# Optimization experiments

Hardware: AMD Instinct MI355X
Metric: run time of the kernel (lower is better)

Reference implementation:

```python
import jax, jax.numpy as jnp
import numpy as np

B, L, K, D = 1024, 8, 16, 64
_KSCALE = 1.0 / np.sqrt(K * D)  # keep channel roughly norm-preserving over layers


def setup_inputs() -> dict:
    key = jax.random.key(0)
    k1, k2, k3, k4 = jax.random.split(key, 4)
    state_re = jax.random.normal(k1, (B, D, D), dtype=jnp.float32)
    state_im = jax.random.normal(k2, (B, D, D), dtype=jnp.float32)
    kraus_re = jax.random.normal(k3, (L, K, D, D), dtype=jnp.float32) * _KSCALE
    kraus_im = jax.random.normal(k4, (L, K, D, D), dtype=jnp.float32) * _KSCALE
    return {"state_re": state_re, "state_im": state_im,
            "kraus_re": kraus_re, "kraus_im": kraus_im}


def reference(state_re, state_im, kraus_re, kraus_im):
    # rho: [B, d, d] complex density matrices; kraus: [L, K, d, d]
    rho = (state_re + 1j * state_im).astype(jnp.complex64)
    kraus = (kraus_re + 1j * kraus_im).astype(jnp.complex64)

    def layer_step(rho, Kl):
        # Kl: [K, d, d]. output_state = sum_k  K_k @ rho @ K_k^dagger
        tmp = jnp.einsum('kij,bjl->kbil', Kl, rho)            # K_k @ rho
        rho_new = jnp.einsum('kbil,kml->bim', tmp, Kl.conj())  # (...) @ K_k^dagger, summed over k
        return rho_new, None

    rho, _ = jax.lax.scan(layer_step, rho, kraus)
    # return real/imag stacked as float32: [2, B, d, d]
    return jnp.stack([rho.real, rho.imag])
```

## Files before the change

kernel.cpp:

```cpp
#include <hip/hip_runtime.h>
#include <hip/hip_fp16.h>

#define D 64
#define NKR 16
#define NB 1024
#define NL 8

typedef __attribute__((ext_vector_type(8))) _Float16 half8;
typedef __attribute__((ext_vector_type(16))) float f32x16;
typedef __attribute__((ext_vector_type(4))) int i32x4;

static __device__ __forceinline__ half8 neg8(half8 x) {
    i32x4 u = __builtin_bit_cast(i32x4, x);
    u = u ^ (int)0x80008000;
    return __builtin_bit_cast(half8, u);
}

static __device__ __forceinline__ unsigned pkrtz(float a, float b) {
    auto h = __builtin_amdgcn_cvt_pkrtz(a, b);
    return __builtin_bit_cast(unsigned, h);
}

static __device__ __forceinline__ void plswap(unsigned &a, unsigned &b) {
    asm volatile("v_permlane32_swap_b32 %0, %1" : "+v"(a), "+v"(b));
}

union Pack4 { _Float16 h[4]; uint2 u; };
union H8 { unsigned u[4]; uint2 v[2]; half8 h; };

#define MFMA __builtin_amdgcn_mfma_f32_32x32x16_f16


__global__ void kconv_kernel(const float* __restrict__ re, const float* __restrict__ im,
                             _Float16* __restrict__ out) {
    int plane = blockIdx.y;
    int idx = blockIdx.x * blockDim.x + threadIdx.x;
    const float* src = plane ? im : re;
    float4 v = ((const float4*)src)[idx];
    int e = idx * 4;
    int lk = e >> 12;
    int rem = e & 4095;
    int row = rem >> 6, col = rem & 63;
    int ihalf = row >> 5, r31 = row & 31;
    int ks = col >> 4, hl2 = (col >> 3) & 1, c = col & 7;
    Pack4 p;
    p.h[0] = (_Float16)v.x; p.h[1] = (_Float16)v.y;
    p.h[2] = (_Float16)v.z; p.h[3] = (_Float16)v.w;
    size_t off = (size_t)(lk * 2 + plane) * 4096 + ihalf * 2048
               + (2 * ks + hl2) * 256 + r31 * 8 + c;
    *(uint2*)(out + off) = p.u;
}

__global__ void sconv_kernel(const float* __restrict__ re, const float* __restrict__ im,
                             _Float16* __restrict__ out) {
    __shared__ float tile[64][65];
    int b = blockIdx.x;
    int t = threadIdx.x;
    for (int plane = 0; plane < 2; ++plane) {
        const float* src = (plane ? im : re) + (size_t)b * 4096;
        __syncthreads();
        #pragma unroll
        for (int i = 0; i < 16; ++i) {
            int e = t + 256 * i;
            tile[e >> 6][e & 63] = src[e];
        }
        __syncthreads();
        _Float16* o = out + ((size_t)b * 2 + plane) * 4096;
        #pragma unroll
        for (int i = 0; i < 16; ++i) {
            int oi = t + 256 * i;
            int lh = oi >> 11, slot = (oi >> 8) & 7, r = (oi >> 3) & 31, c = oi & 7;
            int col = 16 * (slot >> 1) + 8 * (slot & 1) + c;
            int row = 32 * lh + r;
            o[oi] = (_Float16)tile[col][row];
        }
    }
}

static __device__ __forceinline__ void exchange(const f32x16 &dd, half8 &f0, half8 &f1) {
    unsigned A0 = pkrtz(dd[0],  dd[1]),  B0 = pkrtz(dd[2],  dd[3]);
    unsigned A1 = pkrtz(dd[4],  dd[5]),  B1 = pkrtz(dd[6],  dd[7]);
    unsigned A2 = pkrtz(dd[8],  dd[9]),  B2 = pkrtz(dd[10], dd[11]);
    unsigned A3 = pkrtz(dd[12], dd[13]), B3 = pkrtz(dd[14], dd[15]);
    plswap(A0, A1);
    plswap(B0, B1);
    plswap(A2, A3);
    plswap(B2, B3);
    H8 h0; h0.u[0] = A0; h0.u[1] = B0; h0.u[2] = A1; h0.u[3] = B1; f0 = h0.h;
    H8 h1; h1.u[0] = A2; h1.u[1] = B2; h1.u[2] = A3; h1.u[3] = B3; f1 = h1.h;
}

template<int IT>
static __device__ __forceinline__ void kstep(
    const _Float16* __restrict__ kb,
    const _Float16* __restrict__ rb,
    f32x16 (&accRe)[2], f32x16 (&accIm)[2],
    int lane)
{
    const _Float16* bo = kb + IT * 2048;
    const _Float16* bx = kb + (1 - IT) * 2048;

    half8 bre[4], bim[4];
    #pragma unroll
    for (int ks = 0; ks < 4; ++ks) {
        bre[ks] = *(const half8*)(bo + ks * 512 + lane * 8);
        bim[ks] = *(const half8*)(bo + 4096 + ks * 512 + lane * 8);
    }

    half8 ar0 = *(const half8*)(rb + lane * 8);
    half8 ai0 = *(const half8*)(rb + 4096 + lane * 8);
    half8 ar1 = *(const half8*)(rb + 2048 + lane * 8);
    half8 ai1 = *(const half8*)(rb + 6144 + lane * 8);

    f32x16 dre0, dim0, dre1, dim1;
    #pragma unroll
    for (int i = 0; i < 16; ++i) { dre0[i] = 0.f; dim0[i] = 0.f; dre1[i] = 0.f; dim1[i] = 0.f; }

    __builtin_amdgcn_s_setprio(1);
    #pragma unroll
    for (int ks = 0; ks < 4; ++ks) {
        half8 xr0, xi0, xr1, xi1;
        if (ks < 3) {
            xr0 = *(const half8*)(rb + (ks + 1) * 512 + lane * 8);
            xi0 = *(const half8*)(rb + 4096 + (ks + 1) * 512 + lane * 8);
            xr1 = *(const half8*)(rb + 2048 + (ks + 1) * 512 + lane * 8);
            xi1 = *(const half8*)(rb + 6144 + (ks + 1) * 512 + lane * 8);
        }
        half8 bn = neg8(bim[ks]);
        dre0 = MFMA(ar0, bre[ks], dre0, 0, 0, 0);
        dre1 = MFMA(ar1, bre[ks], dre1, 0, 0, 0);
        dim0 = MFMA(ar0, bim[ks], dim0, 0, 0, 0);
        dim1 = MFMA(ar1, bim[ks], dim1, 0, 0, 0);
        dre0 = MFMA(ai0, bn, dre0, 0, 0, 0);
        dre1 = MFMA(ai1, bn, dre1, 0, 0, 0);
        dim0 = MFMA(ai0, bre[ks], dim0, 0, 0, 0);
        dim1 = MFMA(ai1, bre[ks], dim1, 0, 0, 0);
        if (ks < 3) { ar0 = xr0; ai0 = xi0; ar1 = xr1; ai1 = xi1; }
    }
    __builtin_amdgcn_s_setprio(0);

    half8 br2[4], bi2[4];
    #pragma unroll
    for (int ks = 0; ks < 4; ++ks) {
        br2[ks] = *(const half8*)(bx + ks * 512 + lane * 8);
        bi2[ks] = *(const half8*)(bx + 4096 + ks * 512 + lane * 8);
    }

    half8 afr[4], afi[4];
    exchange(dre0, afr[0], afr[1]);
    exchange(dre1, afr[2], afr[3]);
    exchange(dim0, afi[0], afi[1]);
    exchange(dim1, afi[2], afi[3]);

    __builtin_amdgcn_s_setprio(1);
    #pragma unroll
    for (int ks = 0; ks < 4; ++ks) {
        half8 an = neg8(afr[ks]);
        accRe[IT]     = MFMA(afr[ks], bre[ks], accRe[IT],     0, 0, 0);
        accIm[IT]     = MFMA(afi[ks], bre[ks], accIm[IT],     0, 0, 0);
        accRe[1 - IT] = MFMA(afr[ks], br2[ks], accRe[1 - IT], 0, 0, 0);
        accIm[1 - IT] = MFMA(afi[ks], br2[ks], accIm[1 - IT], 0, 0, 0);
        accRe[IT]     = MFMA(afi[ks], bim[ks], accRe[IT],     0, 0, 0);
        accIm[IT]     = MFMA(an,      bim[ks], accIm[IT],     0, 0, 0);
        accRe[1 - IT] = MFMA(afi[ks], bi2[ks], accRe[1 - IT], 0, 0, 0);
        accIm[1 - IT] = MFMA(an,      bi2[ks], accIm[1 - IT], 0, 0, 0);
    }
    __builtin_amdgcn_s_setprio(0);
}

template<int IT>
static __device__ __forceinline__ void run_layer(
    const _Float16* __restrict__ kraus,
    const _Float16* __restrict__ rb,
    f32x16 (&accRe)[2], f32x16 (&accIm)[2],
    int lane)
{
    #pragma unroll 1
    for (int k = 0; k < NKR; ++k)
        kstep<IT>(kraus + (size_t)k * 8192, rb, accRe, accIm, lane);
}

__global__ __launch_bounds__(64, 2) void layer_kernel(
    const _Float16* __restrict__ rho_in,
    _Float16* __restrict__ rho_out,
    float* __restrict__ final_out,
    const _Float16* __restrict__ kraus,
    int last)
{
    const int b    = blockIdx.x;
    const int IT   = blockIdx.y;
    const int lane = threadIdx.x;
    const int l31  = lane & 31;
    const int hl   = lane >> 5;

    const _Float16* rb = rho_in + (size_t)b * 2 * D * D;

    f32x16 accRe[2], accIm[2];
    #pragma unroll
    for (int mt = 0; mt < 2; ++mt)
        #pragma unroll
        for (int i = 0; i < 16; ++i) { accRe[mt][i] = 0.f; accIm[mt][i] = 0.f; }

    if (IT == 0) run_layer<0>(kraus, rb, accRe, accIm, lane);
    else         run_layer<1>(kraus, rb, accRe, accIm, lane);

    if (!last) {
        _Float16* ob = rho_out + (size_t)b * 2 * D * D;
        #pragma unroll
        for (int mt = 0; mt < 2; ++mt) {
            #pragma unroll
            for (int g = 0; g < 4; ++g) {
                Pack4 pr, pi;
                #pragma unroll
                for (int j = 0; j < 4; ++j) {
                    pr.h[j] = (_Float16)accRe[mt][4 * g + j];
                    pi.h[j] = (_Float16)accIm[mt][4 * g + j];
                }
                const int off = mt * 2048 + (4 * IT + g) * 256 + l31 * 8 + 4 * hl;
                *(uint2*)(ob + off)        = pr.u;
                *(uint2*)(ob + 4096 + off) = pi.u;
            }
        }
    } else {
        float* o0 = final_out + (size_t)b * 4096;
        float* o1 = final_out + (size_t)(NB + b) * 4096;
        #pragma unroll
        for (int mt = 0; mt < 2; ++mt) {
            const int m = 32 * mt + l31;
            #pragma unroll
            for (int g = 0; g < 4; ++g) {
                #pragma unroll
                for (int j = 0; j < 4; ++j) {
                    const int i = 32 * IT + 8 * g + 4 * hl + j;
                    o0[i * D + m] = accRe[mt][4 * g + j];
                    o1[i * D + m] = accIm[mt][4 * g + j];
                }
            }
        }
    }
}

extern "C" void kernel_launch(void* const* d_in, const int* in_sizes, int n_in,
                              void* d_out, int out_size, void* d_ws, size_t ws_size,
                              hipStream_t stream) {
    const float* state_re = (const float*)d_in[0];
    const float* state_im = (const float*)d_in[1];
    const float* kraus_re = (const float*)d_in[2];
    const float* kraus_im = (const float*)d_in[3];

    _Float16* kraus_h = (_Float16*)d_ws;
    _Float16* bufA = (_Float16*)d_out;
    _Float16* bufB = (_Float16*)((char*)d_out + (size_t)NB * 2 * D * D * sizeof(_Float16));
    float* fout = (float*)d_out;

    kconv_kernel<<<dim3(512, 2), 256, 0, stream>>>(kraus_re, kraus_im, kraus_h);
    sconv_kernel<<<NB, 256, 0, stream>>>(state_re, state_im, bufA);

    for (int l = 0; l < NL; ++l) {
        const _Float16* in = (l & 1) ? bufB : bufA;
        _Float16* out      = (l & 1) ? bufA : bufB;
        layer_kernel<<<dim3(NB, 2), 64, 0, stream>>>(in, out, fout,
                                                     kraus_h + (size_t)l * NKR * 2 * D * D,
                                                     (l == NL - 1) ? 1 : 0);
    }
}
```

Before: 589.0 us.

## Stage rho tile in LDS shared by two waves per block

Merges the two per-batch wavefronts (previously separate blocks along grid y) into one 128-thread block. The 16 KB fp16 rho tile is copied into LDS once with global_load_lds, and each Kraus step reads it from LDS instead of re-reading global memory 16 times. All four K-slices of rho fragments are now loaded up front rather than prefetched one at a time. This cuts redundant global/L2 traffic for rho. In exchange it adds LDS usage, a block barrier, and higher register pressure, which may lower occupancy.

Measured after the change: 554.5 us. 1.06x faster.

```diff
diff --git a/kernel.cpp b/kernel.cpp
--- a/kernel.cpp
+++ b/kernel.cpp
@@ -27,6 +27,10 @@
 
 union Pack4 { _Float16 h[4]; uint2 u; };
 union H8 { unsigned u[4]; uint2 v[2]; half8 h; };
+
+#define GLDS16(gp, lp) \
+    __builtin_amdgcn_global_load_lds((const __attribute__((address_space(1))) void*)(gp), \
+                                     (__attribute__((address_space(3))) void*)(lp), 16, 0, 0)
 
 #define MFMA __builtin_amdgcn_mfma_f32_32x32x16_f16
 
@@ -93,7 +97,7 @@
 template<int IT>
 static __device__ __forceinline__ void kstep(
     const _Float16* __restrict__ kb,
-    const _Float16* __restrict__ rb,
+    const _Float16* __restrict__ rl,
     f32x16 (&accRe)[2], f32x16 (&accIm)[2],
     int lane)
 {
@@ -107,10 +111,14 @@
         bim[ks] = *(const half8*)(bo + 4096 + ks * 512 + lane * 8);
     }
 
-    half8 ar0 = *(const half8*)(rb + lane * 8);
-    half8 ai0 = *(const half8*)(rb + 4096 + lane * 8);
-    half8 ar1 = *(const half8*)(rb + 2048 + lane * 8);
-    half8 ai1 = *(const half8*)(rb + 6144 + lane * 8);
+    half8 ar0[4], ai0[4], ar1[4], ai1[4];
+    #pragma unroll
+    for (int ks = 0; ks < 4; ++ks) {
+        ar0[ks] = *(const half8*)(rl + ks * 512 + lane * 8);
+        ai0[ks] = *(const half8*)(rl + 4096 + ks * 512 + lane * 8);
+        ar1[ks] = *(const half8*)(rl + 2048 + ks * 512 + lane * 8);
+        ai1[ks] = *(const half8*)(rl + 6144 + ks * 512 + lane * 8);
+    }
 
     f32x16 dre0, dim0, dre1, dim1;
     #pragma unroll
@@ -119,23 +127,15 @@
     __builtin_amdgcn_s_setprio(1);
     #pragma unroll
     for (int ks = 0; ks < 4; ++ks) {
-        half8 xr0, xi0, xr1, xi1;
-        if (ks < 3) {
-            xr0 = *(const half8*)(rb + (ks + 1) * 512 + lane * 8);
-            xi0 = *(const half8*)(rb + 4096 + (ks + 1) * 512 + lane * 8);
-            xr1 = *(const half8*)(rb + 2048 + (ks + 1) * 512 + lane * 8);
-            xi1 = *(const half8*)(rb + 6144 + (ks + 1) * 512 + lane * 8);
-        }
         half8 bn = neg8(bim[ks]);
-        dre0 = MFMA(ar0, bre[ks], dre0, 0, 0, 0);
-        dre1 = MFMA(ar1, bre[ks], dre1, 0, 0, 0);
-        dim0 = MFMA(ar0, bim[ks], dim0, 0, 0, 0);
-        dim1 = MFMA(ar1, bim[ks], dim1, 0, 0, 0);
-        dre0 = MFMA(ai0, bn, dre0, 0, 0, 0);
-        dre1 = MFMA(ai1, bn, dre1, 0, 0, 0);
-        dim0 = MFMA(ai0, bre[ks], dim0, 0, 0, 0);
-        dim1 = MFMA(ai1, bre[ks], dim1, 0, 0, 0);
-        if (ks < 3) { ar0 = xr0; ai0 = xi0; ar1 = xr1; ai1 = xi1; }
+        dre0 = MFMA(ar0[ks], bre[ks], dre0, 0, 0, 0);
+        dre1 = MFMA(ar1[ks], bre[ks], dre1, 0, 0, 0);
+        dim0 = MFMA(ar0[ks], bim[ks], dim0, 0, 0, 0);
+        dim1 = MFMA(ar1[ks], bim[ks], dim1, 0, 0, 0);
+        dre0 = MFMA(ai0[ks], bn, dre0, 0, 0, 0);
+        dre1 = MFMA(ai1[ks], bn, dre1, 0, 0, 0);
+        dim0 = MFMA(ai0[ks], bre[ks], dim0, 0, 0, 0);
+        dim1 = MFMA(ai1[ks], bre[ks], dim1, 0, 0, 0);
     }
     __builtin_amdgcn_s_setprio(0);
 
@@ -171,29 +171,38 @@
 template<int IT>
 static __device__ __forceinline__ void run_layer(
     const _Float16* __restrict__ kraus,
-    const _Float16* __restrict__ rb,
+    const _Float16* __restrict__ rl,
     f32x16 (&accRe)[2], f32x16 (&accIm)[2],
     int lane)
 {
     #pragma unroll 1
     for (int k = 0; k < NKR; ++k)
-        kstep<IT>(kraus + (size_t)k * 8192, rb, accRe, accIm, lane);
-}
-
-__global__ __launch_bounds__(64, 2) void layer_kernel(
+        kstep<IT>(kraus + (size_t)k * 8192, rl, accRe, accIm, lane);
+}
+
+__global__ __launch_bounds__(128, 2) void layer_kernel(
     const _Float16* __restrict__ rho_in,
     _Float16* __restrict__ rho_out,
     float* __restrict__ final_out,
     const _Float16* __restrict__ kraus,
     int last)
 {
+    __shared__ __align__(16) _Float16 Rlds[2 * D * D];
+
     const int b    = blockIdx.x;
-    const int IT   = blockIdx.y;
-    const int lane = threadIdx.x;
+    const int t    = threadIdx.x;
+    const int IT   = t >> 6;
+    const int lane = t & 63;
     const int l31  = lane & 31;
     const int hl   = lane >> 5;
 
-    const _Float16* rb = rho_in + (size_t)b * 2 * D * D;
+    {
+        const char* rb = (const char*)(rho_in + (size_t)b * 2 * D * D);
+        const int off = IT * 8192;
+        #pragma unroll
+        for (int r = 0; r < 8; ++r)
+            GLDS16(rb + off + r * 1024 + lane * 16, (char*)Rlds + off + r * 1024);
+    }
 
     f32x16 accRe[2], accIm[2];
     #pragma unroll
@@ -201,8 +210,10 @@
         #pragma unroll
         for (int i = 0; i < 16; ++i) { accRe[mt][i] = 0.f; accIm[mt][i] = 0.f; }
 
-    if (IT == 0) run_layer<0>(kraus, rb, accRe, accIm, lane);
-    else         run_layer<1>(kraus, rb, accRe, accIm, lane);
+    __syncthreads();
+
+    if (IT == 0) run_layer<0>(kraus, Rlds, accRe, accIm, lane);
+    else         run_layer<1>(kraus, Rlds, accRe, accIm, lane);
 
     if (!last) {
         _Float16* ob = rho_out + (size_t)b * 2 * D * D;
@@ -259,8 +270,8 @@
     for (int l = 0; l < NL; ++l) {
         const _Float16* in = (l & 1) ? bufB : bufA;
         _Float16* out      = (l & 1) ? bufA : bufB;
-        layer_kernel<<<dim3(NB, 2), 64, 0, stream>>>(in, out, fout,
-                                                     kraus_h + (size_t)l * NKR * 2 * D * D,
-                                                     (l == NL - 1) ? 1 : 0);
-    }
-}
+        layer_kernel<<<NB, 128, 0, stream>>>(in, out, fout,
+                                             kraus_h + (size_t)l * NKR * 2 * D * D,
+                                             (l == NL - 1) ? 1 : 0);
+    }
+}
```
